# Performance work log

Measured on AMD Instinct MI355X. Metric: run time of the kernel, lower is better.

Reference implementation:

```python
import jax, jax.numpy as jnp
import numpy as np
from jax import lax

N_QUBITS = 10
N_LAYERS = 6
DIM = 1 << N_QUBITS
EPS = 1e-5

_i = np.arange(DIM)
# Z_SIGNS[w, i] = (+1/-1) eigenvalue of PauliZ on wire w (wire 0 = most significant bit)
Z_SIGNS = jnp.asarray(np.stack([1.0 - 2.0 * ((_i >> (N_QUBITS - 1 - w)) & 1) for w in range(N_QUBITS)]).astype(np.float32))

def _layer_perm(r):
    # composed permutation of the ring of CNOT(w, (w+r)%n) gates of one StronglyEntanglingLayers layer
    p = _i.copy()
    for w in range(N_QUBITS):
        c, t = w, (w + r) % N_QUBITS
        pc, pt = N_QUBITS - 1 - c, N_QUBITS - 1 - t
        pg = _i ^ (((_i >> pc) & 1) << pt)
        p = p[pg]
    return p

LAYER_PERMS = [jnp.asarray(_layer_perm(l % (N_QUBITS - 1) + 1), dtype=jnp.int32) for l in range(N_LAYERS)]

def _apply_1q(state, U, wire):
    # state: (B, DIM) complex64; U: (2,2) or batched (B,2,2)
    B = state.shape[0]
    left = 1 << wire
    right = DIM // (2 * left)
    s = state.reshape(B, left, 2, right)
    if U.ndim == 3:
        out = jnp.einsum('bij,bljr->blir', U, s)
    else:
        out = jnp.einsum('ij,bljr->blir', U, s)
    return out.reshape(B, DIM)

def _ry_batched(theta):
    c = jnp.cos(theta / 2)
    s = jnp.sin(theta / 2)
    return jnp.stack([jnp.stack([c, -s], -1), jnp.stack([s, c], -1)], -2).astype(jnp.complex64)

def _rot(phi, theta, omega):
    # PennyLane Rot(phi, theta, omega) = RZ(omega) @ RY(theta) @ RZ(phi)
    c = jnp.cos(theta / 2)
    s = jnp.sin(theta / 2)
    m00 = jnp.exp(-1j * (phi + omega) / 2) * c
    m01 = -jnp.exp(1j * (phi - omega) / 2) * s
    m10 = jnp.exp(-1j * (phi - omega) / 2) * s
    m11 = jnp.exp(1j * (phi + omega) / 2) * c
    return jnp.stack([jnp.stack([m00, m01]), jnp.stack([m10, m11])]).astype(jnp.complex64)

def quantum_forward(xq, qw):
    # batched statevector simulation of: RY(pi*x_i) encoding + StronglyEntanglingLayers
    B = xq.shape[0]
    state = jnp.zeros((B, DIM), jnp.complex64).at[:, 0].set(1.0)
    for w in range(N_QUBITS):
        state = _apply_1q(state, _ry_batched(jnp.pi * xq[:, w]), w)
    for l in range(N_LAYERS):
        for w in range(N_QUBITS):
            state = _apply_1q(state, _rot(qw[l, w, 0], qw[l, w, 1], qw[l, w, 2]), w)
        state = state[:, LAYER_PERMS[l]]
    probs = state.real ** 2 + state.imag ** 2
    return probs @ Z_SIGNS.T  # (B, N_QUBITS) expvals of PauliZ

def _conv(x, w, b):
    y = lax.conv_general_dilated(x, w, (1, 1), 'SAME', dimension_numbers=('NCHW', 'OIHW', 'NCHW'))
    return y + b[None, :, None, None]

def _bn(x, g, b):
    # BatchNorm2d in training mode: per-batch statistics over (N, H, W)
    m = jnp.mean(x, (0, 2, 3), keepdims=True)
    v = jnp.var(x, (0, 2, 3), keepdims=True)
    return (x - m) * lax.rsqrt(v + EPS) * g[None, :, None, None] + b[None, :, None, None]

def _pool(x):
    return lax.reduce_window(x, -jnp.inf, lax.max, (1, 1, 2, 2), (1, 1, 2, 2), 'VALID')

def setup_inputs() -> dict:
    key = jax.random.key(0)
    ks = jax.random.split(key, 16)
    n = lambda k, sh, sc: jax.random.normal(k, sh, jnp.float32) * sc
    return {
        'x': jax.random.normal(ks[0], (256, 3, 64, 64), jnp.float32),
        'conv1_w': n(ks[1], (32, 3, 3, 3), 0.1), 'conv1_b': jnp.zeros(32),
        'bn1_g': jnp.ones(32), 'bn1_b': jnp.zeros(32),
        'conv2_w': n(ks[2], (32, 32, 3, 3), 0.05), 'conv2_b': jnp.zeros(32),
        'bn2_g': jnp.ones(32), 'bn2_b': jnp.zeros(32),
        'conv3_w': n(ks[3], (64, 32, 3, 3), 0.05), 'conv3_b': jnp.zeros(64),
        'bn3_g': jnp.ones(64), 'bn3_b': jnp.zeros(64),
        'conv4_w': n(ks[4], (64, 64, 3, 3), 0.05), 'conv4_b': jnp.zeros(64),
        'bn4_g': jnp.ones(64), 'bn4_b': jnp.zeros(64),
        'fc1_w': n(ks[5], (128, 64 * 16 * 16), 0.01), 'fc1_b': jnp.zeros(128),
        'fc2_w': n(ks[6], (10, 128), 0.05), 'fc2_b': jnp.zeros(10),
        'q_weights': jax.random.uniform(ks[7], (6, 10, 3), jnp.float32),
        'head_w': n(ks[8], (10, 10), 0.1), 'head_b': jnp.zeros(10),
    }

def reference(x, conv1_w, conv1_b, bn1_g, bn1_b, conv2_w, conv2_b, bn2_g, bn2_b,
              conv3_w, conv3_b, bn3_g, bn3_b, conv4_w, conv4_b, bn4_g, bn4_b,
              fc1_w, fc1_b, fc2_w, fc2_b, q_weights, head_w, head_b):
    h = jax.nn.relu(_bn(_conv(x, conv1_w, conv1_b), bn1_g, bn1_b))
    h = jax.nn.relu(_bn(_conv(h, conv2_w, conv2_b), bn2_g, bn2_b))
    h = _pool(h)  # Dropout(0.25) is identity in eval
    h = jax.nn.relu(_bn(_conv(h, conv3_w, conv3_b), bn3_g, bn3_b))
    h = jax.nn.relu(_bn(_conv(h, conv4_w, conv4_b), bn4_g, bn4_b))
    h = _pool(h)
    h = h.reshape(h.shape[0], -1)  # (B, 64*16*16)
    h = jax.nn.relu(h @ fc1_w.T + fc1_b)
    h = h @ fc2_w.T + fc2_b  # (B, n_qubits)
    q = quantum_forward(h, q_weights)
    return q @ head_w.T + head_b  # (B, num_classes)
```

## Files before the change

kernel.cpp:

```cpp
#include <hip/hip_runtime.h>
#include <math.h>

#define PI_F 3.14159265358979323846f

typedef __attribute__((ext_vector_type(8))) _Float16 half8;
typedef __attribute__((ext_vector_type(4))) _Float16 half4;
typedef __attribute__((ext_vector_type(4))) float f32x4;

__global__ __launch_bounds__(256) void x_to_nhwc4_kernel(
    const float* __restrict__ x, _Float16* __restrict__ X4)
{
    int idx = blockIdx.x * 256 + threadIdx.x;
    int n = idx >> 11;
    int p = (idx & 2047) * 2;
    const float* xb = x + (size_t)n * 12288;
    float2 c0 = *(const float2*)&xb[p];
    float2 c1 = *(const float2*)&xb[4096 + p];
    float2 c2 = *(const float2*)&xb[8192 + p];
    half8 o;
    o[0] = (_Float16)c0.x; o[1] = (_Float16)c1.x; o[2] = (_Float16)c2.x; o[3] = (_Float16)0.f;
    o[4] = (_Float16)c0.y; o[5] = (_Float16)c1.y; o[6] = (_Float16)c2.y; o[7] = (_Float16)0.f;
    *(half8*)&X4[(size_t)idx * 8] = o;
}

__global__ __launch_bounds__(256) void wt_transform_kernel(
    const float* __restrict__ w1, const float* __restrict__ w2,
    const float* __restrict__ w3, const float* __restrict__ w4,
    _Float16* __restrict__ t1, _Float16* __restrict__ t2,
    _Float16* __restrict__ t3, _Float16* __restrict__ t4)
{
    int idx = blockIdx.x * 256 + threadIdx.x;
    if (idx < 9216) {
        int j = idx & 7, co = (idx >> 3) & 31, k8 = idx >> 8;
        int k = k8 * 8 + j, tap = k >> 5, ci = k & 31;
        t2[idx] = (_Float16)w2[(size_t)(co * 32 + ci) * 9 + tap];
    } else if (idx < 27648) {
        int e = idx - 9216;
        int j = e & 7, co = (e >> 3) & 31, r = e >> 8;
        int k8 = r % 36, gg = r / 36;
        int k = k8 * 8 + j, tap = k >> 5, ci = k & 31;
        t3[e] = (_Float16)w3[(size_t)((gg * 32 + co) * 32 + ci) * 9 + tap];
    } else if (idx < 64512) {
        int e = idx - 27648;
        int j = e & 7, co = (e >> 3) & 31, r = e >> 8;
        int k8 = r % 36, gc = r / 36;
        int g = gc >> 1, cc = gc & 1;
        int kl = k8 * 8 + j, tap = kl >> 5, ci = cc * 32 + (kl & 31);
        t4[e] = (_Float16)w4[(size_t)((g * 32 + co) * 64 + ci) * 9 + tap];
    } else if (idx < 66560) {
        int e = idx - 64512;
        int j = e & 7, co = (e >> 3) & 31, k8 = e >> 8;
        int k = k8 * 8 + j, tap = k >> 2, ci = k & 3;
        t1[e] = (_Float16)((tap < 9 && ci < 3) ? w1[(size_t)(co * 3 + ci) * 9 + tap] : 0.f);
    }
}

__global__ __launch_bounds__(256) void fc1w_transform_kernel(
    const float* __restrict__ w, _Float16* __restrict__ wt)
{
    __shared__ float lds[64][65];
    const int t = threadIdx.x;
    const int yx0 = blockIdx.x * 64;
    const int j = blockIdx.y;
    #pragma unroll
    for (int i = 0; i < 16; ++i) {
        int idx = t + 256 * i;
        int c = idx >> 6, yxl = idx & 63;
        lds[c][yxl] = w[(size_t)j * 16384 + c * 256 + yx0 + yxl];
    }
    __syncthreads();
    #pragma unroll
    for (int i = 0; i < 2; ++i) {
        int idx = t + 256 * i;
        int yxl = idx >> 3, c8 = idx & 7;
        half8 h;
        #pragma unroll
        for (int jj = 0; jj < 8; ++jj)
            h[jj] = (_Float16)lds[c8 * 8 + jj][yxl];
        *(half8*)&wt[(size_t)j * 16384 + (size_t)(yx0 + yxl) * 64 + c8 * 8] = h;
    }
}

__global__ __launch_bounds__(256) void quantum_prep_kernel(
    const float* __restrict__ qw, float* __restrict__ rotm,
    unsigned short* __restrict__ perm)
{
    int t = threadIdx.x;
    if (t < 60) {
        float phi = qw[t * 3], th = qw[t * 3 + 1], om = qw[t * 3 + 2];
        float c = cosf(0.5f * th), s = sinf(0.5f * th);
        float apo = 0.5f * (phi + om), amo = 0.5f * (phi - om);
        float cpo = cosf(apo), spo = sinf(apo);
        float cmo = cosf(amo), smo = sinf(amo);
        rotm[t * 8 + 0] = cpo * c;  rotm[t * 8 + 1] = -spo * c;
        rotm[t * 8 + 2] = -cmo * s; rotm[t * 8 + 3] = -smo * s;
        rotm[t * 8 + 4] = cmo * s;  rotm[t * 8 + 5] = -smo * s;
        rotm[t * 8 + 6] = cpo * c;  rotm[t * 8 + 7] = spo * c;
    }
    for (int e = t; e < 6144; e += 256) {
        int layer = e >> 10, i = e & 1023;
        int r = layer % 9 + 1;
        int jdx = i;
        for (int w = 9; w >= 0; --w) {
            int tt = (w + r) % 10;
            int pc = 9 - w, pt_ = 9 - tt;
            jdx ^= ((jdx >> pc) & 1) << pt_;
        }
        perm[e] = (unsigned short)jdx;
    }
}

__global__ __launch_bounds__(256) void conv1_mfma_kernel(
    const _Float16* __restrict__ X4, const _Float16* __restrict__ w1m,
    const float* __restrict__ bias, _Float16* __restrict__ out,
    float* __restrict__ partials)
{
    constexpr int TC = 66, TR = 6;
    constexpr int NPIX = (TR + 1) * TC;
    __shared__ __align__(16) _Float16 s_in[NPIX * 4];
    __shared__ __align__(16) _Float16 s_w[2048];
    __shared__ float s_red[64];

    const int t = threadIdx.x;
    const int row0 = blockIdx.x * 4;
    const int n = blockIdx.z;

    *(half8*)&s_w[t * 8] = *(const half8*)&w1m[t * 8];

    for (int p = t; p < NPIX; p += 256) {
        int col = p % TC, r = p / TC;
        int gy = row0 + r - 1, gx = col - 1;
        uint2 u = make_uint2(0u, 0u);
        if (r < TR && gy >= 0 && gy < 64 && gx >= 0 && gx < 64)
            u = *(const uint2*)&X4[(((size_t)n << 12) + (gy << 6) + gx) * 4];
        *(uint2*)&s_in[p * 4] = u;
    }
    if (t < 64) s_red[t] = 0.f;
    __syncthreads();

    const int w = t >> 6, l = t & 63;
    const int lm = l & 15, lg = l >> 4;
    int pA[4];
    #pragma unroll
    for (int f = 0; f < 4; ++f) {
        int m = w * 64 + f * 16 + lm;
        pA[f] = (m >> 6) * TC + (m & 63);
    }
    f32x4 zero4 = {0.f, 0.f, 0.f, 0.f};
    f32x4 acc[4][2];
    #pragma unroll
    for (int f = 0; f < 4; ++f) { acc[f][0] = zero4; acc[f][1] = zero4; }

    {
        const int t0 = lg * 2;
        const int off0 = (t0 / 3) * TC + (t0 % 3);
        const int off1 = ((t0 + 1) / 3) * TC + ((t0 + 1) % 3);
        half8 b0 = *(const half8*)&s_w[(lg * 32 + lm) * 8];
        half8 b1 = *(const half8*)&s_w[(lg * 32 + 16 + lm) * 8];
        #pragma unroll
        for (int f = 0; f < 4; ++f) {
            half4 alo = *(const half4*)&s_in[(pA[f] + off0) * 4];
            half4 ahi = *(const half4*)&s_in[(pA[f] + off1) * 4];
            half8 a;
            #pragma unroll
            for (int j = 0; j < 4; ++j) { a[j] = alo[j]; a[4 + j] = ahi[j]; }
            acc[f][0] = __builtin_amdgcn_mfma_f32_16x16x32_f16(a, b0, acc[f][0], 0, 0, 0);
            acc[f][1] = __builtin_amdgcn_mfma_f32_16x16x32_f16(a, b1, acc[f][1], 0, 0, 0);
        }
    }
    {
        half8 b0 = *(const half8*)&s_w[((4 + lg) * 32 + lm) * 8];
        half8 b1 = *(const half8*)&s_w[((4 + lg) * 32 + 16 + lm) * 8];
        #pragma unroll
        for (int f = 0; f < 4; ++f) {
            half8 a;
            #pragma unroll
            for (int j = 0; j < 8; ++j) a[j] = (_Float16)0.f;
            if (lg == 0) {
                half4 alo = *(const half4*)&s_in[(pA[f] + 134) * 4];
                half4 ahi = *(const half4*)&s_in[(pA[f] + 198) * 4];
                #pragma unroll
                for (int j = 0; j < 4; ++j) { a[j] = alo[j]; a[4 + j] = ahi[j]; }
            }
            acc[f][0] = __builtin_amdgcn_mfma_f32_16x16x32_f16(a, b0, acc[f][0], 0, 0, 0);
            acc[f][1] = __builtin_amdgcn_mfma_f32_16x16x32_f16(a, b1, acc[f][1], 0, 0, 0);
        }
    }

    float bv0 = bias[lm];
    float bv1 = bias[16 + lm];
    float s0 = 0.f, s20 = 0.f, s1 = 0.f, s21 = 0.f;
    #pragma unroll
    for (int f = 0; f < 4; ++f) {
        #pragma unroll
        for (int r = 0; r < 4; ++r) {
            int m = w * 64 + f * 16 + lg * 4 + r;
            int yy = row0 + (m >> 6), xo = m & 63;
            size_t base = (((size_t)n * 64 + yy) * 64 + xo) * 32;
            float v0 = acc[f][0][r] + bv0;
            float v1 = acc[f][1][r] + bv1;
            out[base + lm] = (_Float16)v0;
            out[base + 16 + lm] = (_Float16)v1;
            s0 += v0; s20 += v0 * v0;
            s1 += v1; s21 += v1 * v1;
        }
    }
    s0 += __shfl_xor(s0, 16);  s0 += __shfl_xor(s0, 32);
    s1 += __shfl_xor(s1, 16);  s1 += __shfl_xor(s1, 32);
    s20 += __shfl_xor(s20, 16); s20 += __shfl_xor(s20, 32);
    s21 += __shfl_xor(s21, 16); s21 += __shfl_xor(s21, 32);
    if (l < 16) {
        atomicAdd(&s_red[lm], s0);
        atomicAdd(&s_red[16 + lm], s1);
        atomicAdd(&s_red[32 + lm], s20);
        atomicAdd(&s_red[48 + lm], s21);
    }
    __syncthreads();
    if (t < 64)
        partials[((size_t)n * 16 + blockIdx.x) * 64 + t] = s_red[t];
}

template<int BLOCK, int W, int CIN, int COUT, int MF, int NB,
         bool MMIN, bool POOL>
__global__ __launch_bounds__(BLOCK, (BLOCK == 512 ? 4 : 3)) void conv_mfma_kernel(
    const _Float16* __restrict__ in0, const _Float16* __restrict__ in1,
    const _Float16* __restrict__ coef, const _Float16* __restrict__ wt,
    const float* __restrict__ bias,
    _Float16* __restrict__ out0, _Float16* __restrict__ out1,
    float* __restrict__ partials)
{
    constexpr int H = W;
    constexpr int NWAVE = BLOCK / 64;
    constexpr int SPW = MF * 16;
    constexpr int ROWS = NWAVE * SPW / W;
    constexpr int TR = ROWS + 2;
    constexpr int TC = W + 2;
    constexpr int NPIX = TR * TC;
    constexpr int NCH = CIN / 32;
    constexpr int C8N = CIN / 8;
    constexpr int KC = 288;
    constexpr int COUTB = NB * 16;
    __shared__ __align__(16) _Float16 s_in[NPIX * CIN];
    __shared__ float s_red[2 * COUTB];

    const int t = threadIdx.x;
    const int row0 = blockIdx.x * ROWS;
    const int n = blockIdx.z;

    const int w = t >> 6, l = t & 63;
    const int lm = l & 15, lg = l >> 4;
    int pA[MF];
    #pragma unroll
    for (int f = 0; f < MF; ++f) {
        int m = w * SPW + f * 16 + lm;
        pA[f] = (m / W) * TC + (m % W);
    }
    f32x4 zero4 = {0.f, 0.f, 0.f, 0.f};
    f32x4 acc[MF][NB];
    #pragma unroll
    for (int f = 0; f < MF; ++f)
        #pragma unroll
        for (int nb = 0; nb < NB; ++nb) acc[f][nb] = zero4;
    if (t < 2 * COUTB) s_red[t] = 0.f;

    for (int idx = t; idx < NPIX * C8N; idx += BLOCK) {
        int c8 = idx % C8N;
        int p = idx / C8N;
        int col = p % TC, r = p / TC;
        int gy = row0 + r - 1, gx = col - 1;
        half8 v;
        #pragma unroll
        for (int j = 0; j < 8; ++j) v[j] = (_Float16)0.f;
        if (gy >= 0 && gy < H && gx >= 0 && gx < W) {
            size_t gidx = (((size_t)n * H + gy) * W + gx) * CIN + c8 * 8;
            if (MMIN) {
                half8 mn = *(const half8*)&in0[gidx];
                half8 mx = *(const half8*)&in1[gidx];
                half8 sa = *(const half8*)&coef[c8 * 8];
                half8 sb = *(const half8*)&coef[CIN + c8 * 8];
                half8 sh = *(const half8*)&coef[2 * CIN + c8 * 8];
                #pragma unroll
                for (int j = 0; j < 8; ++j) {
                    _Float16 f = mx[j] * sa[j] + mn[j] * sb[j] + sh[j];
                    v[j] = f > (_Float16)0.f ? f : (_Float16)0.f;
                }
            } else {
                v = *(const half8*)&in0[gidx];
                if (coef) {
                    half8 sc = *(const half8*)&coef[c8 * 8];
                    half8 sh = *(const half8*)&coef[CIN + c8 * 8];
                    #pragma unroll
                    for (int j = 0; j < 8; ++j) {
                        _Float16 f = v[j] * sc[j] + sh[j];
                        v[j] = f > (_Float16)0.f ? f : (_Float16)0.f;
                    }
                }
            }
        }
        *(half8*)&s_in[(c8 * NPIX + p) * 8] = v;
    }
    __syncthreads();

    #pragma unroll
    for (int tap = 0; tap < 9; ++tap) {
        const int dy = tap / 3, dx = tap % 3;
        const int poff = dy * TC + dx;
        #pragma unroll
        for (int cc = 0; cc < NCH; ++cc) {
            half8 b[NB];
            #pragma unroll
            for (int nb = 0; nb < NB; ++nb) {
                int cog = nb * 16 + lm;
                int gg = cog >> 5, col = cog & 31;
                const _Float16* wp = wt + (size_t)(gg * NCH + cc) * KC * 32;
                b[nb] = *(const half8*)&wp[((tap * 4 + lg) * 32 + col) * 8];
            }
            #pragma unroll
            for (int f = 0; f < MF; ++f) {
                half8 a = *(const half8*)&s_in[((cc * 4 + lg) * NPIX + pA[f] + poff) * 8];
                #pragma unroll
                for (int nb = 0; nb < NB; ++nb)
                    acc[f][nb] = __builtin_amdgcn_mfma_f32_16x16x32_f16(a, b[nb], acc[f][nb], 0, 0, 0);
            }
        }
    }

    float bv[NB], s[NB], s2[NB];
    #pragma unroll
    for (int nb = 0; nb < NB; ++nb) {
        bv[nb] = bias[nb * 16 + lm];
        s[nb] = 0.f; s2[nb] = 0.f;
    }
    #pragma unroll
    for (int f = 0; f < MF; ++f) {
        #pragma unroll
        for (int r = 0; r < 4; ++r) {
            int m = w * SPW + f * 16 + lg * 4 + r;
            int yy = row0 + m / W, xo = m % W;
            size_t base = (((size_t)n * H + yy) * W + xo) * COUT;
            #pragma unroll
            for (int nb = 0; nb < NB; ++nb) {
                float v = acc[f][nb][r] + bv[nb];
                if (!POOL) out0[base + nb * 16 + lm] = (_Float16)v;
                s[nb] += v; s2[nb] += v * v;
            }
        }
    }
    #pragma unroll
    for (int nb = 0; nb < NB; ++nb) {
        s[nb] += __shfl_xor(s[nb], 16);  s[nb] += __shfl_xor(s[nb], 32);
        s2[nb] += __shfl_xor(s2[nb], 16); s2[nb] += __shfl_xor(s2[nb], 32);
    }
    if (l < 16) {
        #pragma unroll
        for (int nb = 0; nb < NB; ++nb) {
            atomicAdd(&s_red[nb * 16 + lm], s[nb]);
            atomicAdd(&s_red[COUTB + nb * 16 + lm], s2[nb]);
        }
    }

    if (POOL) {
        constexpr int FH = MF / 2;
        constexpr int PPIX = (ROWS / 2) * (W / 2);
        static_assert(2 * PPIX * COUT <= NPIX * CIN, "pool pack fits in s_in");
        __syncthreads();
        _Float16* pk = s_in;
        #pragma unroll
        for (int nb = 0; nb < NB; ++nb) {
            #pragma unroll
            for (int f = 0; f < FH; ++f) {
                #pragma unroll
                for (int rp = 0; rp < 2; ++rp) {
                    float a0 = acc[f][nb][2 * rp] + bv[nb];
                    float a1 = acc[f][nb][2 * rp + 1] + bv[nb];
                    float a2 = acc[f + FH][nb][2 * rp] + bv[nb];
                    float a3 = acc[f + FH][nb][2 * rp + 1] + bv[nb];
                    float mn = fminf(fminf(a0, a1), fminf(a2, a3));
                    float mx = fmaxf(fmaxf(a0, a1), fmaxf(a2, a3));
                    int xp = f * 8 + lg * 2 + rp;
                    int o = (w * (W / 2) + xp) * COUT + nb * 16 + lm;
                    pk[o] = (_Float16)mn;
                    pk[PPIX * COUT + o] = (_Float16)mx;
                }
            }
        }
        __syncthreads();
        size_t gb = (((size_t)n * (H / 2) + (row0 >> 1)) * (W / 2)) * COUT;
        for (int idx = t; idx < PPIX * COUT / 8; idx += BLOCK) {
            *(half8*)&out0[gb + (size_t)idx * 8] = *(const half8*)&pk[idx * 8];
            *(half8*)&out1[gb + (size_t)idx * 8] = *(const half8*)&pk[(PPIX * COUT + idx * 8)];
        }
    }

    __syncthreads();
    if (t < 2 * COUTB) {
        size_t bid = (size_t)n * gridDim.x + blockIdx.x;
        partials[bid * 2 * COUTB + t] = s_red[t];
    }
}

__global__ __launch_bounds__(256) void bn_finalize_kernel(
    const float* __restrict__ partials, int nx, float inv_count,
    const float* __restrict__ gamma, const float* __restrict__ beta,
    float* __restrict__ ss, _Float16* __restrict__ ssh,
    _Float16* __restrict__ sab, int COUT)
{
    const int c = blockIdx.x;
    const int t = threadIdx.x;
    float sum = 0.f, sq = 0.f;
    int total = 256 * nx;
    for (int e = t; e < total; e += 256) {
        size_t off = (size_t)e * 2 * COUT;
        sum += partials[off + c];
        sq  += partials[off + COUT + c];
    }
    #pragma unroll
    for (int off = 32; off > 0; off >>= 1) {
        sum += __shfl_xor(sum, off);
        sq  += __shfl_xor(sq, off);
    }
    __shared__ float rs[4], rq[4];
    if ((t & 63) == 0) { rs[t >> 6] = sum; rq[t >> 6] = sq; }
    __syncthreads();
    if (t == 0) {
        sum = rs[0] + rs[1] + rs[2] + rs[3];
        sq  = rq[0] + rq[1] + rq[2] + rq[3];
        float mean = sum * inv_count;
        float var = sq * inv_count - mean * mean;
        float scale = gamma[c] * rsqrtf(var + 1e-5f);
        float shift = beta[c] - mean * scale;
        ss[c] = scale;
        ss[COUT + c] = shift;
        if (ssh) {
            ssh[c] = (_Float16)scale;
            ssh[COUT + c] = (_Float16)shift;
        }
        if (sab) {
            sab[c] = (_Float16)(scale > 0.f ? scale : 0.f);
            sab[COUT + c] = (_Float16)(scale > 0.f ? 0.f : scale);
            sab[2 * COUT + c] = (_Float16)shift;
        }
    }
}

__global__ __launch_bounds__(256) void fc1_mfma_kernel(
    const _Float16* __restrict__ Amin, const _Float16* __restrict__ Amax,
    const _Float16* __restrict__ sab, const _Float16* __restrict__ Bw,
    float* __restrict__ hp)
{
    __shared__ __align__(16) _Float16 As[64][72];
    __shared__ __align__(16) _Float16 Bs[128][72];
    const int t = threadIdx.x;
    const int mt = blockIdx.x;
    const int kc = blockIdx.y;
    const int w = t >> 6, l = t & 63;
    const int lm = l & 15, lg = l >> 4;

    f32x4 zero4 = {0.f, 0.f, 0.f, 0.f};
    f32x4 acc[8];
    #pragma unroll
    for (int nb = 0; nb < 8; ++nb) acc[nb] = zero4;

    const size_t a_base = (size_t)(mt * 64) * 16384 + (size_t)kc * 512;
    const size_t b_base = (size_t)kc * 512;

    for (int p = 0; p < 8; ++p) {
        __syncthreads();
        #pragma unroll
        for (int i = 0; i < 2; ++i) {
            int idx = t + 256 * i;
            int r = idx >> 3, c8 = idx & 7;
            size_t off = a_base + (size_t)r * 16384 + p * 64 + c8 * 8;
            half8 mn = *(const half8*)&Amin[off];
            half8 mx = *(const half8*)&Amax[off];
            half8 sa = *(const half8*)&sab[c8 * 8];
            half8 sb = *(const half8*)&sab[64 + c8 * 8];
            half8 sh = *(const half8*)&sab[128 + c8 * 8];
            half8 v;
            #pragma unroll
            for (int j = 0; j < 8; ++j) {
                _Float16 f = mx[j] * sa[j] + mn[j] * sb[j] + sh[j];
                v[j] = f > (_Float16)0.f ? f : (_Float16)0.f;
            }
            *(half8*)&As[r][c8 * 8] = v;
        }
        #pragma unroll
        for (int i = 0; i < 4; ++i) {
            int idx = t + 256 * i;
            int r = idx >> 3, c8 = idx & 7;
            *(half8*)&Bs[r][c8 * 8] =
                *(const half8*)&Bw[b_base + (size_t)r * 16384 + p * 64 + c8 * 8];
        }
        __syncthreads();
        #pragma unroll
        for (int ks = 0; ks < 64; ks += 32) {
            half8 a = *(const half8*)&As[w * 16 + lm][ks + lg * 8];
            #pragma unroll
            for (int nb = 0; nb < 8; ++nb) {
                half8 b = *(const half8*)&Bs[nb * 16 + lm][ks + lg * 8];
                acc[nb] = __builtin_amdgcn_mfma_f32_16x16x32_f16(a, b, acc[nb], 0, 0, 0);
            }
        }
    }
    #pragma unroll
    for (int nb = 0; nb < 8; ++nb) {
        #pragma unroll
        for (int r = 0; r < 4; ++r) {
            int row = mt * 64 + w * 16 + lg * 4 + r;
            hp[((size_t)kc * 256 + row) * 128 + nb * 16 + lm] = acc[nb][r];
        }
    }
}

__global__ __launch_bounds__(256) void fc1_reduce_kernel(
    const float* __restrict__ hp, const float* __restrict__ bias, float* __restrict__ h1)
{
    int gid = blockIdx.x * 256 + threadIdx.x;
    int n = gid >> 7, j = gid & 127;
    float s = bias[j];
    #pragma unroll
    for (int kc = 0; kc < 32; ++kc) s += hp[((size_t)kc * 256 + n) * 128 + j];
    h1[gid] = fmaxf(0.f, s);
}

__global__ __launch_bounds__(64) void fc2_kernel(
    const float* __restrict__ h1, const float* __restrict__ w,
    const float* __restrict__ b, float* __restrict__ xq)
{
    int n = blockIdx.x, l = threadIdx.x;
    float a0 = h1[n * 128 + l], a1 = h1[n * 128 + 64 + l];
    float p[10];
    #pragma unroll
    for (int j = 0; j < 10; ++j)
        p[j] = w[j * 128 + l] * a0 + w[j * 128 + 64 + l] * a1;
    #pragma unroll
    for (int j = 0; j < 10; ++j) {
        #pragma unroll
        for (int off = 32; off > 0; off >>= 1) p[j] += __shfl_xor(p[j], off);
    }
    if (l == 0) {
        #pragma unroll
        for (int j = 0; j < 10; ++j) xq[n * 10 + j] = p[j] + b[j];
    }
}

__global__ __launch_bounds__(64) void quantum_head_kernel(
    const float* __restrict__ xq, const float* __restrict__ rotm,
    const unsigned short* __restrict__ perm,
    const float* __restrict__ head_w, const float* __restrict__ head_b,
    float* __restrict__ outp)
{
    __shared__ float lds[2048];
    const int n = blockIdx.x;
    const int l = threadIdx.x;

    float ar[16], ai[16];
    #pragma unroll
    for (int r = 0; r < 16; ++r) { ar[r] = 0.f; ai[r] = 0.f; }
    if (l == 0) ar[0] = 1.f;

    #pragma unroll
    for (int w = 0; w < 10; ++w) {
        float th = 0.5f * PI_F * xq[n * 10 + w];
        float c = cosf(th), s = sinf(th);
        const int k = 9 - w;
        if (k >= 6) {
            const int b = k - 6;
            #pragma unroll
            for (int r = 0; r < 16; ++r) {
                if (!(r & (1 << b))) {
                    int r1 = r | (1 << b);
                    float a0 = ar[r], a1 = ar[r1];
                    ar[r]  = c * a0 - s * a1;
                    ar[r1] = s * a0 + c * a1;
                }
            }
        } else {
            float ss = ((l >> k) & 1) ? s : -s;
            #pragma unroll
            for (int r = 0; r < 16; ++r) {
                float p = __shfl_xor(ar[r], 1 << k);
                ar[r] = c * ar[r] + ss * p;
            }
        }
    }

    #pragma unroll 1
    for (int layer = 0; layer < 6; ++layer) {
        #pragma unroll
        for (int w = 0; w < 10; ++w) {
            const float* m = rotm + (layer * 10 + w) * 8;
            float m00r = m[0], m00i = m[1], m01r = m[2], m01i = m[3];
            float m10r = m[4], m10i = m[5], m11r = m[6], m11i = m[7];
            const int k = 9 - w;
            if (k >= 6) {
                const int b = k - 6;
                #pragma unroll
                for (int r = 0; r < 16; ++r) {
                    if (!(r & (1 << b))) {
                        int r1 = r | (1 << b);
                        float a0r = ar[r], a0i = ai[r];
                        float a1r = ar[r1], a1i = ai[r1];
                        ar[r]  = m00r * a0r - m00i * a0i + m01r * a1r - m01i * a1i;
                        ai[r]  = m00r * a0i + m00i * a0r + m01r * a1i + m01i * a1r;
                        ar[r1] = m10r * a0r - m10i * a0i + m11r * a1r - m11i * a1i;
                        ai[r1] = m10r * a0i + m10i * a0r + m11r * a1i + m11i * a1r;
                    }
                }
            } else {
                int bit = (l >> k) & 1;
                float mAr = bit ? m11r : m00r, mAi = bit ? m11i : m00i;
                float mBr = bit ? m10r : m01r, mBi = bit ? m10i : m01i;
                #pragma unroll
                for (int r = 0; r < 16; ++r) {
                    float pr = __shfl_xor(ar[r], 1 << k);
                    float pi = __shfl_xor(ai[r], 1 << k);
                    float mr = ar[r], mi = ai[r];
                    ar[r] = mAr * mr - mAi * mi + mBr * pr - mBi * pi;
                    ai[r] = mAr * mi + mAi * mr + mBr * pi + mBi * pr;
                }
            }
        }
        #pragma unroll
        for (int r = 0; r < 16; ++r) {
            lds[(r << 6) | l] = ar[r];
            lds[1024 + ((r << 6) | l)] = ai[r];
        }
        __syncthreads();
        const unsigned short* pt = perm + layer * 1024;
        #pragma unroll
        for (int r = 0; r < 16; ++r) {
            int ji = pt[(r << 6) | l];
            ar[r] = lds[ji];
            ai[r] = lds[1024 + ji];
        }
        __syncthreads();
    }

    float S = 0.f, T0 = 0.f, T1 = 0.f, T2 = 0.f, T3 = 0.f;
    #pragma unroll
    for (int r = 0; r < 16; ++r) {
        float pr = ar[r] * ar[r] + ai[r] * ai[r];
        S += pr;
        T0 += (r & 1) ? -pr : pr;
        T1 += (r & 2) ? -pr : pr;
        T2 += (r & 4) ? -pr : pr;
        T3 += (r & 8) ? -pr : pr;
    }
    float pk[10];
    pk[0] = T3; pk[1] = T2; pk[2] = T1; pk[3] = T0;
    #pragma unroll
    for (int w = 4; w < 10; ++w)
        pk[w] = ((l >> (9 - w)) & 1) ? -S : S;
    #pragma unroll
    for (int w = 0; w < 10; ++w) {
        #pragma unroll
        for (int off = 1; off < 64; off <<= 1)
            pk[w] += __shfl_xor(pk[w], off);
    }
    if (l < 10) {
        float o = head_b[l];
        #pragma unroll
        for (int kk = 0; kk < 10; ++kk) o += pk[kk] * head_w[l * 10 + kk];
        outp[n * 10 + l] = o;
    }
}

extern "C" void kernel_launch(void* const* d_in, const int* in_sizes, int n_in,
                              void* d_out, int out_size, void* d_ws, size_t ws_size,
                              hipStream_t stream)
{
    const float* x   = (const float*)d_in[0];
    const float* c1w = (const float*)d_in[1];  const float* c1b = (const float*)d_in[2];
    const float* g1  = (const float*)d_in[3];  const float* b1  = (const float*)d_in[4];
    const float* c2w = (const float*)d_in[5];  const float* c2b = (const float*)d_in[6];
    const float* g2  = (const float*)d_in[7];  const float* b2  = (const float*)d_in[8];
    const float* c3w = (const float*)d_in[9];  const float* c3b = (const float*)d_in[10];
    const float* g3  = (const float*)d_in[11]; const float* b3  = (const float*)d_in[12];
    const float* c4w = (const float*)d_in[13]; const float* c4b = (const float*)d_in[14];
    const float* g4  = (const float*)d_in[15]; const float* b4  = (const float*)d_in[16];
    const float* f1w = (const float*)d_in[17]; const float* f1b = (const float*)d_in[18];
    const float* f2w = (const float*)d_in[19]; const float* f2b = (const float*)d_in[20];
    const float* qw  = (const float*)d_in[21];
    const float* hw  = (const float*)d_in[22]; const float* hb  = (const float*)d_in[23];

    float* ws = (float*)d_ws;
    _Float16* H0 = (_Float16*)ws;
    _Float16* H1 = H0 + 33554432;
    float* part = ws + 33554432;
    float* ss1  = part + 524288;
    float* ss2  = ss1 + 64;
    float* ss3  = ss2 + 64;
    float* ss4  = ss3 + 128;
    float* hp   = ss4 + 128;
    float* h1   = hp + 1048576;
    float* xqv  = h1 + 32768;
    float* rotm = xqv + 2560;
    unsigned short* perm16 = (unsigned short*)(rotm + 480);
    _Float16* ssh1 = (_Float16*)(perm16 + 6144);
    _Float16* ssh3 = ssh1 + 64;
    _Float16* sab2 = ssh3 + 128;
    _Float16* sab4 = sab2 + 96;
    _Float16* wt2  = sab4 + 192;
    _Float16* wt3  = wt2 + 9216;
    _Float16* wt4  = wt3 + 18432;
    _Float16* w1m  = wt4 + 36864;
    _Float16* w1t  = w1m + 2048;
    _Float16* X4   = w1t + 2097152;

    _Float16* minT2 = H1;
    _Float16* maxT2 = H1 + 8388608;
    _Float16* minT4 = H1;
    _Float16* maxT4 = H1 + 4194304;

    quantum_prep_kernel<<<1, 256, 0, stream>>>(qw, rotm, perm16);
    wt_transform_kernel<<<260, 256, 0, stream>>>(c1w, c2w, c3w, c4w, w1m, wt2, wt3, wt4);
    fc1w_transform_kernel<<<dim3(4, 128), 256, 0, stream>>>(f1w, w1t);
    x_to_nhwc4_kernel<<<2048, 256, 0, stream>>>(x, X4);

    conv1_mfma_kernel<<<dim3(16, 1, 256), 256, 0, stream>>>(X4, w1m, c1b, H0, part);
    bn_finalize_kernel<<<32, 256, 0, stream>>>(part, 16, 1.f / 1048576.f,
                                               g1, b1, ss1, ssh1, nullptr, 32);

    conv_mfma_kernel<256, 64, 32, 32, 8, 2, false, true>
        <<<dim3(8, 1, 256), 256, 0, stream>>>(
        H0, nullptr, ssh1, wt2, c2b, minT2, maxT2, part);
    bn_finalize_kernel<<<32, 256, 0, stream>>>(part, 8, 1.f / 1048576.f,
                                               g2, b2, ss2, nullptr, sab2, 32);

    conv_mfma_kernel<512, 32, 32, 64, 4, 4, true, false>
        <<<dim3(2, 1, 256), 512, 0, stream>>>(
        minT2, maxT2, sab2, wt3, c3b, H0, nullptr, part);
    bn_finalize_kernel<<<64, 256, 0, stream>>>(part, 2, 1.f / 262144.f,
                                               g3, b3, ss3, ssh3, nullptr, 64);

    conv_mfma_kernel<512, 32, 64, 64, 4, 4, false, true>
        <<<dim3(2, 1, 256), 512, 0, stream>>>(
        H0, nullptr, ssh3, wt4, c4b, minT4, maxT4, part);
    bn_finalize_kernel<<<64, 256, 0, stream>>>(part, 2, 1.f / 262144.f,
                                               g4, b4, ss4, nullptr, sab4, 64);

    fc1_mfma_kernel<<<dim3(4, 32), 256, 0, stream>>>(minT4, maxT4, sab4, w1t, hp);
    fc1_reduce_kernel<<<128, 256, 0, stream>>>(hp, f1b, h1);

    fc2_kernel<<<256, 64, 0, stream>>>(h1, f2w, f2b, xqv);

    quantum_head_kernel<<<256, 64, 0, stream>>>(xqv, rotm, perm16, hw, hb, (float*)d_out);
}
```

Baseline: 203.0 us.

## Recompute conv1 inside conv2 instead of storing conv1 activations

Conv1 now runs only to collect BatchNorm statistics and no longer writes its fp16 output to global memory. The conv2 kernel recomputes conv1 on its haloed tile from the 4-channel input, then applies BN1 and ReLU into shared memory before running conv2. This removes a large global write and read of the 32-channel intermediate. The cost is conv1 being computed twice, including halo rows, plus more shared memory per block, which can lower occupancy.

```diff
diff --git a/kernel.cpp b/kernel.cpp
--- a/kernel.cpp
+++ b/kernel.cpp
@@ -110,10 +110,9 @@
     }
 }
 
-__global__ __launch_bounds__(256) void conv1_mfma_kernel(
+__global__ __launch_bounds__(256) void conv1_stats_kernel(
     const _Float16* __restrict__ X4, const _Float16* __restrict__ w1m,
-    const float* __restrict__ bias, _Float16* __restrict__ out,
-    float* __restrict__ partials)
+    const float* __restrict__ bias, float* __restrict__ partials)
 {
     constexpr int TC = 66, TR = 6;
     constexpr int NPIX = (TR + 1) * TC;
@@ -194,13 +193,8 @@
     for (int f = 0; f < 4; ++f) {
         #pragma unroll
         for (int r = 0; r < 4; ++r) {
-            int m = w * 64 + f * 16 + lg * 4 + r;
-            int yy = row0 + (m >> 6), xo = m & 63;
-            size_t base = (((size_t)n * 64 + yy) * 64 + xo) * 32;
             float v0 = acc[f][0][r] + bv0;
             float v1 = acc[f][1][r] + bv1;
-            out[base + lm] = (_Float16)v0;
-            out[base + 16 + lm] = (_Float16)v1;
             s0 += v0; s20 += v0 * v0;
             s1 += v1; s21 += v1 * v1;
         }
@@ -218,6 +212,205 @@
     __syncthreads();
     if (t < 64)
         partials[((size_t)n * 16 + blockIdx.x) * 64 + t] = s_red[t];
+}
+
+__global__ __launch_bounds__(256, 2) void conv2_fused_kernel(
+    const _Float16* __restrict__ X4, const _Float16* __restrict__ w1m,
+    const float* __restrict__ c1bias, const _Float16* __restrict__ ssh1,
+    const _Float16* __restrict__ wt2, const float* __restrict__ c2bias,
+    _Float16* __restrict__ out0, _Float16* __restrict__ out1,
+    float* __restrict__ partials)
+{
+    constexpr int W = 64, COUT = 32, MF = 8, NB = 2;
+    constexpr int SPW = MF * 16;
+    constexpr int ROWS = 8;
+    constexpr int TR = 10, TC = 66, NPIX = TR * TC;
+    constexpr int KC = 288;
+    constexpr int XC = 68, XROWS = 14, XPIX = XROWS * XC;
+    __shared__ __align__(16) _Float16 s_in[NPIX * 32];
+    __shared__ __align__(16) _Float16 s_x4[XPIX * 4];
+    __shared__ __align__(16) _Float16 s_w1[2048];
+    __shared__ float s_red[64];
+
+    const int t = threadIdx.x;
+    const int row0 = blockIdx.x * ROWS;
+    const int n = blockIdx.z;
+    const int w = t >> 6, l = t & 63;
+    const int lm = l & 15, lg = l >> 4;
+
+    *(half8*)&s_w1[t * 8] = *(const half8*)&w1m[t * 8];
+    for (int p = t; p < XPIX; p += 256) {
+        int c = p % XC, r = p / XC;
+        int gy = row0 - 2 + r, gx = c - 2;
+        uint2 u = make_uint2(0u, 0u);
+        if (r < 12 && gy >= 0 && gy < 64 && gx >= 0 && gx < 64)
+            u = *(const uint2*)&X4[(((size_t)n << 12) + (gy << 6) + gx) * 4];
+        *(uint2*)&s_x4[p * 4] = u;
+    }
+    if (t < 64) s_red[t] = 0.f;
+    __syncthreads();
+
+    {
+        const float b1v0 = c1bias[lm], b1v1 = c1bias[16 + lm];
+        const _Float16 sc0 = ssh1[lm], sh0 = ssh1[32 + lm];
+        const _Float16 sc1 = ssh1[16 + lm], sh1 = ssh1[48 + lm];
+        const int c8a = lm >> 3, ja = lm & 7;
+        for (int g = w; g < 42; g += 4) {
+            int py = g * 16 + lm;
+            int ry = py / 66, cy = py - ry * 66;
+            int pb = ry * XC + cy;
+            f32x4 a0 = {0.f, 0.f, 0.f, 0.f}, a1 = {0.f, 0.f, 0.f, 0.f};
+            {
+                const int t0 = lg * 2;
+                const int off0 = (t0 / 3) * XC + (t0 % 3);
+                const int off1 = ((t0 + 1) / 3) * XC + ((t0 + 1) % 3);
+                half8 b0 = *(const half8*)&s_w1[(lg * 32 + lm) * 8];
+                half8 b1 = *(const half8*)&s_w1[(lg * 32 + 16 + lm) * 8];
+                half4 alo = *(const half4*)&s_x4[(pb + off0) * 4];
+                half4 ahi = *(const half4*)&s_x4[(pb + off1) * 4];
+                half8 a;
+                #pragma unroll
+                for (int j = 0; j < 4; ++j) { a[j] = alo[j]; a[4 + j] = ahi[j]; }
+                a0 = __builtin_amdgcn_mfma_f32_16x16x32_f16(a, b0, a0, 0, 0, 0);
+                a1 = __builtin_amdgcn_mfma_f32_16x16x32_f16(a, b1, a1, 0, 0, 0);
+            }
+            {
+                half8 b0 = *(const half8*)&s_w1[((4 + lg) * 32 + lm) * 8];
+                half8 b1 = *(const half8*)&s_w1[((4 + lg) * 32 + 16 + lm) * 8];
+                half8 a;
+                #pragma unroll
+                for (int j = 0; j < 8; ++j) a[j] = (_Float16)0.f;
+                if (lg == 0) {
+                    half4 alo = *(const half4*)&s_x4[(pb + 138) * 4];
+                    half4 ahi = *(const half4*)&s_x4[(pb + 204) * 4];
+                    #pragma unroll
+                    for (int j = 0; j < 4; ++j) { a[j] = alo[j]; a[4 + j] = ahi[j]; }
+                }
+                a0 = __builtin_amdgcn_mfma_f32_16x16x32_f16(a, b0, a0, 0, 0, 0);
+                a1 = __builtin_amdgcn_mfma_f32_16x16x32_f16(a, b1, a1, 0, 0, 0);
+            }
+            #pragma unroll
+            for (int r2 = 0; r2 < 4; ++r2) {
+                int py2 = g * 16 + lg * 4 + r2;
+                if (py2 < NPIX) {
+                    int r2y = py2 / 66, c2y = py2 - r2y * 66;
+                    int gy = row0 - 1 + r2y, gx = c2y - 1;
+                    _Float16 y0 = (_Float16)0.f, y1 = (_Float16)0.f;
+                    if (gy >= 0 && gy < 64 && gx >= 0 && gx < 64) {
+                        _Float16 v0 = (_Float16)(a0[r2] + b1v0);
+                        _Float16 v1 = (_Float16)(a1[r2] + b1v1);
+                        _Float16 f0 = v0 * sc0 + sh0;
+                        _Float16 f1 = v1 * sc1 + sh1;
+                        y0 = f0 > (_Float16)0.f ? f0 : (_Float16)0.f;
+                        y1 = f1 > (_Float16)0.f ? f1 : (_Float16)0.f;
+                    }
+                    s_in[(c8a * NPIX + py2) * 8 + ja] = y0;
+                    s_in[((2 + c8a) * NPIX + py2) * 8 + ja] = y1;
+                }
+            }
+        }
+    }
+    __syncthreads();
+
+    int pA[MF];
+    #pragma unroll
+    for (int f = 0; f < MF; ++f) {
+        int m = w * SPW + f * 16 + lm;
+        pA[f] = (m / W) * TC + (m % W);
+    }
+    f32x4 zero4 = {0.f, 0.f, 0.f, 0.f};
+    f32x4 acc[MF][NB];
+    #pragma unroll
+    for (int f = 0; f < MF; ++f)
+        #pragma unroll
+        for (int nb = 0; nb < NB; ++nb) acc[f][nb] = zero4;
+
+    #pragma unroll
+    for (int tap = 0; tap < 9; ++tap) {
+        const int dy = tap / 3, dx = tap % 3;
+        const int poff = dy * TC + dx;
+        half8 b[NB];
+        #pragma unroll
+        for (int nb = 0; nb < NB; ++nb) {
+            int col = nb * 16 + lm;
+            b[nb] = *(const half8*)&wt2[((tap * 4 + lg) * 32 + col) * 8];
+        }
+        #pragma unroll
+        for (int f = 0; f < MF; ++f) {
+            half8 a = *(const half8*)&s_in[(lg * NPIX + pA[f] + poff) * 8];
+            #pragma unroll
+            for (int nb = 0; nb < NB; ++nb)
+                acc[f][nb] = __builtin_amdgcn_mfma_f32_16x16x32_f16(a, b[nb], acc[f][nb], 0, 0, 0);
+        }
+    }
+
+    float bv[NB], s[NB], s2[NB];
+    #pragma unroll
+    for (int nb = 0; nb < NB; ++nb) {
+        bv[nb] = c2bias[nb * 16 + lm];
+        s[nb] = 0.f; s2[nb] = 0.f;
+    }
+    #pragma unroll
+    for (int f = 0; f < MF; ++f) {
+        #pragma unroll
+        for (int r = 0; r < 4; ++r) {
+            #pragma unroll
+            for (int nb = 0; nb < NB; ++nb) {
+                float v = acc[f][nb][r] + bv[nb];
+                s[nb] += v; s2[nb] += v * v;
+            }
+        }
+    }
+    #pragma unroll
+    for (int nb = 0; nb < NB; ++nb) {
+        s[nb] += __shfl_xor(s[nb], 16);  s[nb] += __shfl_xor(s[nb], 32);
+        s2[nb] += __shfl_xor(s2[nb], 16); s2[nb] += __shfl_xor(s2[nb], 32);
+    }
+    if (l < 16) {
+        #pragma unroll
+        for (int nb = 0; nb < NB; ++nb) {
+            atomicAdd(&s_red[nb * 16 + lm], s[nb]);
+            atomicAdd(&s_red[32 + nb * 16 + lm], s2[nb]);
+        }
+    }
+
+    {
+        constexpr int FH = MF / 2;
+        constexpr int PPIX = (ROWS / 2) * (W / 2);
+        __syncthreads();
+        _Float16* pk = s_in;
+        #pragma unroll
+        for (int nb = 0; nb < NB; ++nb) {
+            #pragma unroll
+            for (int f = 0; f < FH; ++f) {
+                #pragma unroll
+                for (int rp = 0; rp < 2; ++rp) {
+                    float a0 = acc[f][nb][2 * rp] + bv[nb];
+                    float a1 = acc[f][nb][2 * rp + 1] + bv[nb];
+                    float a2 = acc[f + FH][nb][2 * rp] + bv[nb];
+                    float a3 = acc[f + FH][nb][2 * rp + 1] + bv[nb];
+                    float mn = fminf(fminf(a0, a1), fminf(a2, a3));
+                    float mx = fmaxf(fmaxf(a0, a1), fmaxf(a2, a3));
+                    int xp = f * 8 + lg * 2 + rp;
+                    int o = (w * (W / 2) + xp) * COUT + nb * 16 + lm;
+                    pk[o] = (_Float16)mn;
+                    pk[PPIX * COUT + o] = (_Float16)mx;
+                }
+            }
+        }
+        __syncthreads();
+        size_t gb = (((size_t)n * 32 + (row0 >> 1)) * 32) * COUT;
+        for (int idx = t; idx < PPIX * COUT / 8; idx += 256) {
+            *(half8*)&out0[gb + (size_t)idx * 8] = *(const half8*)&pk[idx * 8];
+            *(half8*)&out1[gb + (size_t)idx * 8] = *(const half8*)&pk[PPIX * COUT + idx * 8];
+        }
+    }
+
+    __syncthreads();
+    if (t < 64) {
+        size_t bid = (size_t)n * gridDim.x + blockIdx.x;
+        partials[bid * 64 + t] = s_red[t];
+    }
 }
 
 template<int BLOCK, int W, int CIN, int COUT, int MF, int NB,
@@ -718,13 +911,12 @@
     fc1w_transform_kernel<<<dim3(4, 128), 256, 0, stream>>>(f1w, w1t);
     x_to_nhwc4_kernel<<<2048, 256, 0, stream>>>(x, X4);
 
-    conv1_mfma_kernel<<<dim3(16, 1, 256), 256, 0, stream>>>(X4, w1m, c1b, H0, part);
+    conv1_stats_kernel<<<dim3(16, 1, 256), 256, 0, stream>>>(X4, w1m, c1b, part);
     bn_finalize_kernel<<<32, 256, 0, stream>>>(part, 16, 1.f / 1048576.f,
                                                g1, b1, ss1, ssh1, nullptr, 32);
 
-    conv_mfma_kernel<256, 64, 32, 32, 8, 2, false, true>
-        <<<dim3(8, 1, 256), 256, 0, stream>>>(
-        H0, nullptr, ssh1, wt2, c2b, minT2, maxT2, part);
+    conv2_fused_kernel<<<dim3(8, 1, 256), 256, 0, stream>>>(
+        X4, w1m, c1b, ssh1, wt2, c2b, minT2, maxT2, part);
     bn_finalize_kernel<<<32, 256, 0, stream>>>(part, 8, 1.f / 1048576.f,
                                                g2, b2, ss2, nullptr, sab2, 32);
 
```

Measured after the change: 214.6 us. 1.06x slower.
